# Kernel tuning notes

Hardware: AMD Instinct MI355X
Metric: run time of the kernel (lower is better)

Reference implementation:

```python
import jax, jax.numpy as jnp
import numpy as np

DIM = 512
NUM_HEADS = 16
HEAD_DIM = DIM // NUM_HEADS
RES = (32, 32)
SEQ_SCALE = float(np.log(RES[0] * RES[1]))  # seq_length_scale buffer
TABLE = (2 * RES[0] - 1) * (2 * RES[1] - 1)  # 3969
EPS = 1e-12


def setup_inputs() -> dict:
    key = jax.random.key(0)
    ks = jax.random.split(key, 12)
    B, N, C = 8, RES[0] * RES[1], DIM
    s = 0.02
    return {
        "x": jax.random.normal(ks[0], (B, N, C), dtype=jnp.float32),
        "_h": RES[0],
        "_w": RES[1],
        "relative_pos_index": jax.random.randint(ks[1], (N, N), 0, TABLE, dtype=jnp.int32),
        "relative_coords_table": jax.random.uniform(ks[2], (TABLE, 2), dtype=jnp.float32, minval=-1.0, maxval=1.0),
        "qkv_w": jax.random.normal(ks[3], (3 * C, C), dtype=jnp.float32) * s,
        "qkv_b": jnp.zeros((3 * C,), dtype=jnp.float32),
        "proj_w": jax.random.normal(ks[4], (C, C), dtype=jnp.float32) * s,
        "proj_b": jnp.zeros((C,), dtype=jnp.float32),
        "temperature": jnp.full((NUM_HEADS, 1, 1), float(np.log(np.expm1(1.0 / 0.24))), dtype=jnp.float32),
        "query_embedding": jax.random.normal(ks[5], (NUM_HEADS, 1, HEAD_DIM), dtype=jnp.float32) * s,
        "cpb_fc1_w": jax.random.normal(ks[6], (512, 2), dtype=jnp.float32) * s,
        "cpb_fc1_b": jnp.zeros((512,), dtype=jnp.float32),
        "cpb_fc2_w": jax.random.normal(ks[7], (NUM_HEADS, 512), dtype=jnp.float32) * s,
        "cpb_fc2_b": jnp.zeros((NUM_HEADS,), dtype=jnp.float32),
    }


def _l2norm(t):
    # F.normalize(t, dim=-1): x / max(||x||, eps)
    n = jnp.sqrt(jnp.sum(t * t, axis=-1, keepdims=True))
    return t / jnp.maximum(n, EPS)


def reference(x, _h, _w, relative_pos_index, relative_coords_table,
              qkv_w, qkv_b, proj_w, proj_b, temperature, query_embedding,
              cpb_fc1_w, cpb_fc1_b, cpb_fc2_w, cpb_fc2_b):
    B, N, C = x.shape
    H, hd = NUM_HEADS, HEAD_DIM
    # qkv projection -> [B, N, 3H, hd] -> [B, 3H, N, hd]
    qkv = (x @ qkv_w.T + qkv_b).reshape(B, N, 3 * H, hd).transpose(0, 2, 1, 3)
    q, k, v = jnp.split(qkv, 3, axis=1)  # each [B, H, N, hd]
    # CPB MLP relative bias: [T,2] -> [T,H] -> gather -> [H,N,N]
    t = jax.nn.relu(relative_coords_table @ cpb_fc1_w.T + cpb_fc1_b) @ cpb_fc2_w.T + cpb_fc2_b
    rel_bias = t[relative_pos_index].transpose(2, 0, 1)  # [H, N, N]
    # cosine attention with learned softplus temperature and query embedding
    scale = jax.nn.softplus(temperature) * SEQ_SCALE  # [H,1,1]
    qn = (_l2norm(q) + query_embedding[None]) * scale[None]
    kn = _l2norm(k)
    attn = jnp.einsum('bhnd,bhmd->bhnm', qn, kn) + rel_bias[None]
    attn = jax.nn.softmax(attn, axis=-1)
    out = jnp.einsum('bhnm,bhmd->bhnd', attn, v)  # [B,H,N,hd]
    out = out.transpose(0, 2, 1, 3).reshape(B, N, C)
    return out @ proj_w.T + proj_b
```

## Files before the change

### kernel.cpp

```cpp
#include <hip/hip_runtime.h>
#include <cstdint>
#include <cstddef>

typedef _Float16 f16;
typedef _Float16 f16x4 __attribute__((ext_vector_type(4)));
typedef _Float16 f16x8 __attribute__((ext_vector_type(8)));
typedef float f32x4 __attribute__((ext_vector_type(4)));

#define MFMA32(a,b,c) __builtin_amdgcn_mfma_f32_16x16x32_f16((a),(b),(c),0,0,0)
#define MFMA16(a,b,c) __builtin_amdgcn_mfma_f32_16x16x16f16((a),(b),(c),0,0,0)

__device__ __forceinline__ float fexp2(float x) {
#if __has_builtin(__builtin_amdgcn_exp2f)
  return __builtin_amdgcn_exp2f(x);
#else
  return __expf(x * 0.69314718055994531f);
#endif
}

__device__ __forceinline__ void gload_lds16(const f16* g, f16* l) {
  __builtin_amdgcn_global_load_lds(
      (const __attribute__((address_space(1))) unsigned int*)g,
      (__attribute__((address_space(3))) unsigned int*)l, 16, 0, 0);
}

static constexpr size_t OFF_TCPB = 0;
static constexpr size_t OFF_BIAS = 262144;
static constexpr size_t OFF_XHI  = OFF_BIAS + 33554432;
static constexpr size_t OFF_XLO  = OFF_XHI + 8388608;
static constexpr size_t OFF_WHI  = OFF_XLO + 8388608;
static constexpr size_t OFF_WLO  = OFF_WHI + 1572864;
static constexpr size_t OFF_PW   = OFF_WLO + 1572864;
static constexpr size_t OFF_QHI  = OFF_PW  + 524288;
static constexpr size_t OFF_QLO  = OFF_QHI + 8388608;
static constexpr size_t OFF_KHI  = OFF_QLO + 8388608;
static constexpr size_t OFF_KLO  = OFF_KHI + 8388608;
static constexpr size_t OFF_VT   = OFF_KLO + 8388608;
static constexpr size_t OFF_AO   = OFF_VT  + 8388608;

__global__ __launch_bounds__(256) void k_convert(
    const float* __restrict__ x, const float* __restrict__ qw, const float* __restrict__ pwf,
    f16* __restrict__ xhi, f16* __restrict__ xlo,
    f16* __restrict__ whi, f16* __restrict__ pw)
{
  int i = blockIdx.x * 256 + threadIdx.x;
  const float4* src; f16* dh; f16* dl; int j;
  if (i < 1048576)      { j = i;           src = (const float4*)x;   dh = xhi; dl = xlo; }
  else if (i < 1245184) { j = i - 1048576; src = (const float4*)qw;  dh = whi; dl = nullptr; }
  else                  { j = i - 1245184; src = (const float4*)pwf; dh = pw;  dl = nullptr; }
  float4 v = src[j];
  f16x4 h;
  h[0] = (f16)v.x; h[1] = (f16)v.y; h[2] = (f16)v.z; h[3] = (f16)v.w;
  ((f16x4*)dh)[j] = h;
  if (dl) {
    f16x4 l;
    l[0] = (f16)(v.x - (float)h[0]); l[1] = (f16)(v.y - (float)h[1]);
    l[2] = (f16)(v.z - (float)h[2]); l[3] = (f16)(v.w - (float)h[3]);
    ((f16x4*)dl)[j] = l;
  }
}

__global__ __launch_bounds__(256) void k_cpb(
    const float* __restrict__ table, const float* __restrict__ w1, const float* __restrict__ b1,
    const float* __restrict__ w2, const float* __restrict__ b2, float* __restrict__ t_out)
{
  const int r = blockIdx.x * 4 + (threadIdx.x >> 6);
  const int lane = threadIdx.x & 63;
  if (r >= 3969) return;
  const float c0 = table[2*r], c1 = table[2*r+1];
  const int j0 = lane * 8;
  float h[8];
#pragma unroll
  for (int jj = 0; jj < 8; jj++) {
    int j = j0 + jj;
    float v = c0 * w1[2*j] + c1 * w1[2*j+1] + b1[j];
    h[jj] = v > 0.0f ? v : 0.0f;
  }
  float acc[16];
#pragma unroll
  for (int o = 0; o < 16; o++) {
    const float4* wp = (const float4*)(w2 + o*512 + j0);
    float4 a = wp[0], bb = wp[1];
    acc[o] = a.x*h[0] + a.y*h[1] + a.z*h[2] + a.w*h[3]
           + bb.x*h[4] + bb.y*h[5] + bb.z*h[6] + bb.w*h[7];
  }
#pragma unroll
  for (int o = 0; o < 16; o++) {
    float v = acc[o];
    for (int s = 1; s < 64; s <<= 1) v += __shfl_xor(v, s, 64);
    acc[o] = v;
  }
  if (lane == 0) {
#pragma unroll
    for (int o = 0; o < 16; o++)
      t_out[r*16 + o] = (acc[o] + b2[o]) * 1.4426950408889634f;
  }
}

__global__ __launch_bounds__(256) void k_bias(
    const int* __restrict__ idx, const float* __restrict__ t_cpb, f16* __restrict__ bias_t)
{
  int g = blockIdx.x * 256 + threadIdx.x;
  int n = g & 1023, m4 = g >> 10;
  int4 I = *(const int4*)(idx + (size_t)n*1024 + m4*4);
  int ids[4] = {I.x, I.y, I.z, I.w};
  const float4* T = (const float4*)t_cpb;
#pragma unroll
  for (int half = 0; half < 2; half++) {
    float4 R[4][2];
#pragma unroll
    for (int k = 0; k < 4; k++) {
      R[k][0] = T[ids[k]*4 + half*2];
      R[k][1] = T[ids[k]*4 + half*2 + 1];
    }
#pragma unroll
    for (int hh = 0; hh < 8; hh++) {
      int h = half*8 + hh;
      f16x4 o;
#pragma unroll
      for (int k = 0; k < 4; k++)
        o[k] = (f16)(((const float*)&R[k][hh >> 2])[hh & 3]);
      *(f16x4*)(bias_t + (((size_t)h*256 + m4)*1024 + n)*4) = o;
    }
  }
}

__global__ __launch_bounds__(256) void k_qkv(
    const f16* __restrict__ xhi, const f16* __restrict__ xlo,
    const f16* __restrict__ whi,
    const float* __restrict__ qkvb, const float* __restrict__ temp, const float* __restrict__ qe,
    f16* __restrict__ qh_o, f16* __restrict__ kh_o, f16* __restrict__ vt_o)
{
  __shared__ __align__(16) f16 Ah[8][64][8];
  __shared__ __align__(16) f16 Al[8][64][8];
  __shared__ __align__(16) f16 Bh[8][64][8];
  const int tid = threadIdx.x, lane = tid & 63, w = tid >> 6;
  const int rsel = lane & 15, ksel = lane >> 4;
  const int bx = blockIdx.x & 63, by = blockIdx.x >> 6;
  const int m0 = bx << 7, n0 = by << 7;
  const bool SPLIT = (by < 8);

  const size_t aoff = (size_t)(m0 + w*32 + rsel)*512 + ksel*8;
  const size_t boff = (size_t)(n0 + w*32 + rsel)*512 + ksel*8;
  const f16 *gA0 = xhi + aoff,  *gA1 = gA0 + 16*512;
  const f16 *gAl0 = xlo + aoff, *gAl1 = gAl0 + 16*512;
  const f16 *gB0 = whi + boff,  *gB1 = gB0 + 16*512;
  f16 *lA0 = &Ah[2*w][0][0],  *lA1 = &Ah[2*w+1][0][0];
  f16 *lAl0 = &Al[2*w][0][0], *lAl1 = &Al[2*w+1][0][0];
  f16 *lB0 = &Bh[2*w][0][0],  *lB1 = &Bh[2*w+1][0][0];

  const f32x4 zero = {0.f, 0.f, 0.f, 0.f};
  f32x4 acc[4][4];
#pragma unroll
  for (int mt = 0; mt < 4; mt++)
#pragma unroll
    for (int nt = 0; nt < 4; nt++) acc[mt][nt] = zero;

  const int mb4 = (w & 1) * 4, nb4 = (w >> 1) * 4;
  for (int k0 = 0; k0 < 512; k0 += 32) {
    __syncthreads();
    gload_lds16(gA0 + k0, lA0);
    gload_lds16(gA1 + k0, lA1);
    gload_lds16(gB0 + k0, lB0);
    gload_lds16(gB1 + k0, lB1);
    if (SPLIT) {
      gload_lds16(gAl0 + k0, lAl0);
      gload_lds16(gAl1 + k0, lAl1);
    }
    __syncthreads();
    f16x8 bhf[4];
#pragma unroll
    for (int nt = 0; nt < 4; nt++) bhf[nt] = ((const f16x8*)&Bh[nb4+nt][0][0])[lane];
    if (SPLIT) {
#pragma unroll
      for (int mt = 0; mt < 4; mt++) {
        f16x8 ah = ((const f16x8*)&Ah[mb4+mt][0][0])[lane];
        f16x8 al = ((const f16x8*)&Al[mb4+mt][0][0])[lane];
#pragma unroll
        for (int nt = 0; nt < 4; nt++) {
          acc[mt][nt] = MFMA32(al, bhf[nt], acc[mt][nt]);
          acc[mt][nt] = MFMA32(ah, bhf[nt], acc[mt][nt]);
        }
      }
    } else {
#pragma unroll
      for (int mt = 0; mt < 4; mt++) {
        f16x8 ah = ((const f16x8*)&Ah[mb4+mt][0][0])[lane];
#pragma unroll
        for (int nt = 0; nt < 4; nt++)
          acc[mt][nt] = MFMA32(ah, bhf[nt], acc[mt][nt]);
      }
    }
  }

  const int mbase = m0 + (w & 1)*64, nbase = n0 + (w >> 1)*64;
  float bc[4];
#pragma unroll
  for (int nt = 0; nt < 4; nt++) bc[nt] = qkvb[nbase + nt*16 + rsel];
#pragma unroll
  for (int mt = 0; mt < 4; mt++)
#pragma unroll
    for (int nt = 0; nt < 4; nt++)
#pragma unroll
      for (int r = 0; r < 4; r++) acc[mt][nt][r] += bc[nt];

  if (by < 8) {
    const bool ISQ = (by < 4);
#pragma unroll
    for (int pair = 0; pair < 2; pair++) {
      const int h = ((nbase - (ISQ ? 0 : 512)) >> 5) + pair;
      float sc = 0.f, qe0 = 0.f, qe1 = 0.f;
      if (ISQ) {
        sc  = log1pf(__expf(temp[h])) * 10.0f;
        qe0 = qe[h*32 + rsel];
        qe1 = qe[h*32 + 16 + rsel];
      }
      f16* dh = ISQ ? qh_o : kh_o;
#pragma unroll
      for (int mt = 0; mt < 4; mt++) {
        float ss[4];
#pragma unroll
        for (int r = 0; r < 4; r++) {
          float a = acc[mt][2*pair][r], b = acc[mt][2*pair+1][r];
          ss[r] = a*a + b*b;
        }
        for (int s = 1; s < 16; s <<= 1) {
#pragma unroll
          for (int r = 0; r < 4; r++) ss[r] += __shfl_xor(ss[r], s, 64);
        }
#pragma unroll
        for (int r = 0; r < 4; r++) {
          float rn = 1.0f / fmaxf(sqrtf(ss[r]), 1e-12f);
          int m = mbase + mt*16 + ksel*4 + r;
          int b_ = m >> 10, p = m & 1023;
          size_t base = ((size_t)(b_*16 + h)*1024 + p)*32;
          float v0 = acc[mt][2*pair][r] * rn;
          float v1 = acc[mt][2*pair+1][r] * rn;
          if (ISQ) { v0 = (v0 + qe0) * sc; v1 = (v1 + qe1) * sc; }
          dh[base + rsel]      = (f16)v0;
          dh[base + 16 + rsel] = (f16)v1;
        }
      }
    }
  } else {
#pragma unroll
    for (int mt = 0; mt < 4; mt++) {
      int m = mbase + mt*16 + ksel*4;
      int b_ = m >> 10, p = m & 1023;
#pragma unroll
      for (int nt = 0; nt < 4; nt++) {
        int n = nbase + nt*16 + rsel;
        int g = (n - 1024) >> 5, d = n & 31;
        f16x4 pk;
#pragma unroll
        for (int r = 0; r < 4; r++) pk[r] = (f16)acc[mt][nt][r];
        *(f16x4*)(vt_o + ((size_t)(b_*16 + g)*32 + d)*1024 + p) = pk;
      }
    }
  }
}

__global__ __launch_bounds__(256, 4) void k_attn(
    const f16* __restrict__ qhi, const f16* __restrict__ khi, const f16* __restrict__ vt,
    const f16* __restrict__ bias_t,
    f16* __restrict__ po0, f16* __restrict__ po1,
    float2* __restrict__ ml0, float2* __restrict__ ml1)
{
  __shared__ __align__(16) f16 OT[4][32][40];
  const int lane = threadIdx.x & 63, w = threadIdx.x >> 6;
  const int rsel = lane & 15, ksel = lane >> 4;
  const int bid = blockIdx.x;
  const int xcd = bid & 7;
  const int r1 = bid >> 3;
  const int h = ((r1 & 1) << 3) | xcd;
  const int r2 = r1 >> 1;
  const int qt = r2 & 7, split = (r2 >> 3) & 1, b = r2 >> 4;
  const int bh = b*16 + h;
  const int q0 = qt*128 + w*32;
  const int mstart = split * 512;

  f16x8 Qh[2];
#pragma unroll
  for (int c = 0; c < 2; c++)
    Qh[c] = *(const f16x8*)(qhi + ((size_t)bh*1024 + q0 + c*16 + rsel)*32 + ksel*8);

  const char* kb = (const char*)(khi + (size_t)bh*32768);
  const char* vb = (const char*)(vt  + (size_t)bh*32768);
  const char* bb = (const char*)(bias_t + (size_t)h*1048576);
  int kOff = ((mstart + rsel)*32 + ksel*8) * 2;
  int vOff = (rsel*1024 + mstart + ksel*4) * 2;
  int bOff = (((mstart >> 2) + ksel)*1024 + q0 + rsel) * 8;

  f32x4 O[2][2];
  float mi[2], li[2];
#pragma unroll
  for (int c = 0; c < 2; c++) {
    O[c][0] = (f32x4){0.f,0.f,0.f,0.f};
    O[c][1] = (f32x4){0.f,0.f,0.f,0.f};
    mi[c] = -3.0e38f; li[c] = 0.f;
  }

  f16x8 Kn0 = *(const f16x8*)(kb + kOff);
  f16x8 Kn1 = *(const f16x8*)(kb + kOff + 1024);
  kOff += 2048;

  for (int it = 0; it < 16; ++it) {
    f16x8 K0 = Kn0, K1 = Kn1;
    if (it < 15) {
      Kn0 = *(const f16x8*)(kb + kOff);
      Kn1 = *(const f16x8*)(kb + kOff + 1024);
      kOff += 2048;
    }
    f16x4 Va[2][2];
    Va[0][0] = *(const f16x4*)(vb + vOff);
    Va[1][0] = *(const f16x4*)(vb + vOff + 32);
    Va[0][1] = *(const f16x4*)(vb + vOff + 32768);
    Va[1][1] = *(const f16x4*)(vb + vOff + 32800);
    vOff += 64;
    f16x4 Bb[2][2];
    Bb[0][0] = *(const f16x4*)(bb + bOff);
    Bb[0][1] = *(const f16x4*)(bb + bOff + 128);
    Bb[1][0] = *(const f16x4*)(bb + bOff + 32768);
    Bb[1][1] = *(const f16x4*)(bb + bOff + 32896);
    bOff += 65536;

    f32x4 St[2][2];
#pragma unroll
    for (int f = 0; f < 2; f++)
#pragma unroll
      for (int c = 0; c < 2; c++) {
        f32x4 Ci;
#pragma unroll
        for (int r = 0; r < 4; r++) Ci[r] = (float)Bb[f][c][r];
        St[f][c] = MFMA32(f ? K1 : K0, Qh[c], Ci);
      }

    f16x4 P16[2][2];
#pragma unroll
    for (int c = 0; c < 2; c++) {
      float cm = fmaxf(fmaxf(fmaxf(St[0][c][0], St[0][c][1]), fmaxf(St[0][c][2], St[0][c][3])),
                       fmaxf(fmaxf(St[1][c][0], St[1][c][1]), fmaxf(St[1][c][2], St[1][c][3])));
      cm = fmaxf(cm, __shfl_xor(cm, 16, 64));
      cm = fmaxf(cm, __shfl_xor(cm, 32, 64));
      float mn = fmaxf(mi[c], cm);
      float alpha = fexp2(mi[c] - mn);
      mi[c] = mn;
      float rs = 0.f;
#pragma unroll
      for (int f = 0; f < 2; f++)
#pragma unroll
        for (int r = 0; r < 4; r++) {
          float p = fexp2(St[f][c][r] - mn);
          rs += p;
          P16[f][c][r] = (f16)p;
        }
      li[c] = li[c]*alpha + rs;
#pragma unroll
      for (int dt = 0; dt < 2; dt++)
#pragma unroll
        for (int r = 0; r < 4; r++) O[c][dt][r] *= alpha;
    }
#pragma unroll
    for (int c = 0; c < 2; c++)
#pragma unroll
      for (int dt = 0; dt < 2; dt++) {
        O[c][dt] = MFMA16(Va[0][dt], P16[0][c], O[c][dt]);
        O[c][dt] = MFMA16(Va[1][dt], P16[1][c], O[c][dt]);
      }
  }

#pragma unroll
  for (int c = 0; c < 2; c++) {
    li[c] += __shfl_xor(li[c], 16, 64);
    li[c] += __shfl_xor(li[c], 32, 64);
    float inv = 1.0f / li[c];
#pragma unroll
    for (int dt = 0; dt < 2; dt++)
#pragma unroll
      for (int r = 0; r < 4; r++)
        OT[w][c*16 + rsel][dt*16 + ksel*4 + r] = (f16)(O[c][dt][r] * inv);
  }
  f16* po_s = split ? po1 : po0;
  float2* ml_s = split ? ml1 : ml0;
  int row = lane >> 1, half = lane & 1;
  f16x8 o0 = *(const f16x8*)(&OT[w][row][half*16]);
  f16x8 o1 = *(const f16x8*)(&OT[w][row][half*16 + 8]);
  f16* outp = po_s + ((size_t)bh*1024 + q0 + row)*32 + half*16;
  *(f16x8*)outp = o0;
  *(f16x8*)(outp + 8) = o1;
  if (lane < 32) {
    int c = lane >> 4;
    float mm = c ? mi[1] : mi[0];
    float ll = c ? li[1] : li[0];
    ml_s[(size_t)bh*1024 + q0 + lane] = make_float2(mm, ll);
  }
}

__global__ __launch_bounds__(256) void k_merge(
    const f16* __restrict__ po0, const f16* __restrict__ po1,
    const float2* __restrict__ ml0, const float2* __restrict__ ml1,
    f16* __restrict__ ao)
{
  int tid = blockIdx.x * 256 + threadIdx.x;
  int h = tid & 15, q = (tid >> 4) & 1023, b = tid >> 14;
  int bh = b*16 + h;
  size_t rec = (size_t)bh*1024 + q;
  float2 a = ml0[rec], c = ml1[rec];
  float M = fmaxf(a.x, c.x);
  float w0 = a.y * fexp2(a.x - M);
  float w1 = c.y * fexp2(c.x - M);
  float inv = 1.0f / (w0 + w1);
  w0 *= inv; w1 *= inv;
  const f16x8* p0 = (const f16x8*)(po0 + rec*32);
  const f16x8* p1 = (const f16x8*)(po1 + rec*32);
  f16* op = ao + ((size_t)b*1024 + q)*512 + h*32;
#pragma unroll
  for (int i = 0; i < 4; i++) {
    f16x8 x0 = p0[i], x1 = p1[i];
    f16x8 o;
#pragma unroll
    for (int j = 0; j < 8; j++) o[j] = (f16)((float)x0[j]*w0 + (float)x1[j]*w1);
    ((f16x8*)op)[i] = o;
  }
}

__global__ __launch_bounds__(256) void k_proj(
    const f16* __restrict__ A, const f16* __restrict__ Bw,
    const float* __restrict__ pb, float* __restrict__ out)
{
  __shared__ __align__(16) f16 Ah[8][64][8];
  __shared__ __align__(16) f16 Bh[8][64][8];
  const int tid = threadIdx.x, lane = tid & 63, w = tid >> 6;
  const int rsel = lane & 15, ksel = lane >> 4;
  const int bx = blockIdx.x & 63, by = blockIdx.x >> 6;
  const int m0 = bx << 7, n0 = by << 7;
  const f16 *gA0 = A + (size_t)(m0 + w*32 + rsel)*512 + ksel*8,  *gA1 = gA0 + 16*512;
  const f16 *gB0 = Bw + (size_t)(n0 + w*32 + rsel)*512 + ksel*8, *gB1 = gB0 + 16*512;
  f16 *lA0 = &Ah[2*w][0][0], *lA1 = &Ah[2*w+1][0][0];
  f16 *lB0 = &Bh[2*w][0][0], *lB1 = &Bh[2*w+1][0][0];
  const f32x4 zero = {0.f, 0.f, 0.f, 0.f};
  f32x4 acc[4][4];
#pragma unroll
  for (int mt = 0; mt < 4; mt++)
#pragma unroll
    for (int nt = 0; nt < 4; nt++) acc[mt][nt] = zero;
  const int mb4 = (w & 1)*4, nb4 = (w >> 1)*4;
  for (int k0 = 0; k0 < 512; k0 += 32) {
    __syncthreads();
    gload_lds16(gA0 + k0, lA0);
    gload_lds16(gA1 + k0, lA1);
    gload_lds16(gB0 + k0, lB0);
    gload_lds16(gB1 + k0, lB1);
    __syncthreads();
    f16x8 bhf[4];
#pragma unroll
    for (int nt = 0; nt < 4; nt++) bhf[nt] = ((const f16x8*)&Bh[nb4+nt][0][0])[lane];
#pragma unroll
    for (int mt = 0; mt < 4; mt++) {
      f16x8 ah = ((const f16x8*)&Ah[mb4+mt][0][0])[lane];
#pragma unroll
      for (int nt = 0; nt < 4; nt++)
        acc[mt][nt] = MFMA32(ah, bhf[nt], acc[mt][nt]);
    }
  }
  const int mbase = m0 + (w & 1)*64, nbase = n0 + (w >> 1)*64;
  float bc[4];
#pragma unroll
  for (int nt = 0; nt < 4; nt++) bc[nt] = pb[nbase + nt*16 + rsel];
#pragma unroll
  for (int mt = 0; mt < 4; mt++)
#pragma unroll
    for (int nt = 0; nt < 4; nt++)
#pragma unroll
      for (int r = 0; r < 4; r++)
        out[(size_t)(mbase + mt*16 + ksel*4 + r)*512 + nbase + nt*16 + rsel] =
            acc[mt][nt][r] + bc[nt];
}

extern "C" void kernel_launch(void* const* d_in, const int* in_sizes, int n_in,
                              void* d_out, int out_size, void* d_ws, size_t ws_size,
                              hipStream_t stream) {
  const float* x    = (const float*)d_in[0];
  const int*   rpi  = (const int*)d_in[3];
  const float* rct  = (const float*)d_in[4];
  const float* qw   = (const float*)d_in[5];
  const float* qb   = (const float*)d_in[6];
  const float* pwf  = (const float*)d_in[7];
  const float* pbv  = (const float*)d_in[8];
  const float* temp = (const float*)d_in[9];
  const float* qe   = (const float*)d_in[10];
  const float* f1w  = (const float*)d_in[11];
  const float* f1b  = (const float*)d_in[12];
  const float* f2w  = (const float*)d_in[13];
  const float* f2b  = (const float*)d_in[14];

  char* ws = (char*)d_ws;
  float* t_cpb  = (float*)(ws + OFF_TCPB);
  f16* bias_t   = (f16*)(ws + OFF_BIAS);
  f16* xhi = (f16*)(ws + OFF_XHI);
  f16* xlo = (f16*)(ws + OFF_XLO);
  f16* whi = (f16*)(ws + OFF_WHI);
  f16* pw  = (f16*)(ws + OFF_PW);
  f16* qhi = (f16*)(ws + OFF_QHI);
  f16* khi = (f16*)(ws + OFF_KHI);
  f16* vt  = (f16*)(ws + OFF_VT);
  f16* ao  = (f16*)(ws + OFF_AO);
  f16* po0 = (f16*)(ws + OFF_KLO);
  f16* po1 = (f16*)(ws + OFF_XHI);
  float2* ml0 = (float2*)(ws + OFF_XLO);
  float2* ml1 = ml0 + 131072;

  k_convert<<<5120, 256, 0, stream>>>(x, qw, pwf, xhi, xlo, whi, pw);
  k_cpb<<<993, 256, 0, stream>>>(rct, f1w, f1b, f2w, f2b, t_cpb);
  k_bias<<<1024, 256, 0, stream>>>(rpi, t_cpb, bias_t);
  k_qkv<<<768, 256, 0, stream>>>(xhi, xlo, whi, qb, temp, qe, qhi, khi, vt);
  k_attn<<<2048, 256, 0, stream>>>(qhi, khi, vt, bias_t, po0, po1, ml0, ml1);
  k_merge<<<512, 256, 0, stream>>>(po0, po1, ml0, ml1, ao);
  k_proj<<<256, 256, 0, stream>>>(ao, pw, pbv, (float*)d_out);
}
```

Measured before the change: 288.8 us.

## Use two-pass softmax: precompute row max, drop online rescaling

Replaces the online-softmax loop with two passes over the key range. The first pass computes QK^T plus bias only to find the exact row max. The second pass recomputes the scores, exponentiates against that fixed max and accumulates P·V with no per-iteration alpha rescale or cross-lane max shuffles. This removes the serial shuffle/rescale dependency chain, but it doubles the QK MFMAs and the K and bias loads, and it drops the software prefetch of K.

```diff
diff --git a/kernel.cpp b/kernel.cpp
--- a/kernel.cpp
+++ b/kernel.cpp
@@ -286,87 +286,85 @@
 
   const char* kb = (const char*)(khi + (size_t)bh*32768);
   const char* vb = (const char*)(vt  + (size_t)bh*32768);
-  const char* bb = (const char*)(bias_t + (size_t)h*1048576);
-  int kOff = ((mstart + rsel)*32 + ksel*8) * 2;
-  int vOff = (rsel*1024 + mstart + ksel*4) * 2;
-  int bOff = (((mstart >> 2) + ksel)*1024 + q0 + rsel) * 8;
+  const char* bbp = (const char*)(bias_t + (size_t)h*1048576);
+  const int kOff0 = ((mstart + rsel)*32 + ksel*8) * 2;
+  const int vOff0 = (rsel*1024 + mstart + ksel*4) * 2;
+  const int bOff0 = (((mstart >> 2) + ksel)*1024 + q0 + rsel) * 8;
+
+  float mx[2] = {-3.0e38f, -3.0e38f};
+  {
+    int kOff = kOff0, bOff = bOff0;
+    for (int it = 0; it < 16; ++it) {
+      f16x8 K0 = *(const f16x8*)(kb + kOff);
+      f16x8 K1 = *(const f16x8*)(kb + kOff + 1024);
+      f16x4 Bb[2][2];
+      Bb[0][0] = *(const f16x4*)(bbp + bOff);
+      Bb[0][1] = *(const f16x4*)(bbp + bOff + 128);
+      Bb[1][0] = *(const f16x4*)(bbp + bOff + 32768);
+      Bb[1][1] = *(const f16x4*)(bbp + bOff + 32896);
+      kOff += 2048; bOff += 65536;
+#pragma unroll
+      for (int f = 0; f < 2; f++)
+#pragma unroll
+        for (int c = 0; c < 2; c++) {
+          f32x4 Ci;
+#pragma unroll
+          for (int r = 0; r < 4; r++) Ci[r] = (float)Bb[f][c][r];
+          f32x4 St = MFMA32(f ? K1 : K0, Qh[c], Ci);
+          mx[c] = fmaxf(mx[c], fmaxf(fmaxf(St[0], St[1]), fmaxf(St[2], St[3])));
+        }
+    }
+  }
+#pragma unroll
+  for (int c = 0; c < 2; c++) {
+    mx[c] = fmaxf(mx[c], __shfl_xor(mx[c], 16, 64));
+    mx[c] = fmaxf(mx[c], __shfl_xor(mx[c], 32, 64));
+  }
 
   f32x4 O[2][2];
-  float mi[2], li[2];
-#pragma unroll
-  for (int c = 0; c < 2; c++) {
-    O[c][0] = (f32x4){0.f,0.f,0.f,0.f};
-    O[c][1] = (f32x4){0.f,0.f,0.f,0.f};
-    mi[c] = -3.0e38f; li[c] = 0.f;
-  }
-
-  f16x8 Kn0 = *(const f16x8*)(kb + kOff);
-  f16x8 Kn1 = *(const f16x8*)(kb + kOff + 1024);
-  kOff += 2048;
-
-  for (int it = 0; it < 16; ++it) {
-    f16x8 K0 = Kn0, K1 = Kn1;
-    if (it < 15) {
-      Kn0 = *(const f16x8*)(kb + kOff);
-      Kn1 = *(const f16x8*)(kb + kOff + 1024);
-      kOff += 2048;
-    }
-    f16x4 Va[2][2];
-    Va[0][0] = *(const f16x4*)(vb + vOff);
-    Va[1][0] = *(const f16x4*)(vb + vOff + 32);
-    Va[0][1] = *(const f16x4*)(vb + vOff + 32768);
-    Va[1][1] = *(const f16x4*)(vb + vOff + 32800);
-    vOff += 64;
-    f16x4 Bb[2][2];
-    Bb[0][0] = *(const f16x4*)(bb + bOff);
-    Bb[0][1] = *(const f16x4*)(bb + bOff + 128);
-    Bb[1][0] = *(const f16x4*)(bb + bOff + 32768);
-    Bb[1][1] = *(const f16x4*)(bb + bOff + 32896);
-    bOff += 65536;
-
-    f32x4 St[2][2];
-#pragma unroll
-    for (int f = 0; f < 2; f++)
-#pragma unroll
-      for (int c = 0; c < 2; c++) {
-        f32x4 Ci;
-#pragma unroll
-        for (int r = 0; r < 4; r++) Ci[r] = (float)Bb[f][c][r];
-        St[f][c] = MFMA32(f ? K1 : K0, Qh[c], Ci);
-      }
-
-    f16x4 P16[2][2];
-#pragma unroll
-    for (int c = 0; c < 2; c++) {
-      float cm = fmaxf(fmaxf(fmaxf(St[0][c][0], St[0][c][1]), fmaxf(St[0][c][2], St[0][c][3])),
-                       fmaxf(fmaxf(St[1][c][0], St[1][c][1]), fmaxf(St[1][c][2], St[1][c][3])));
-      cm = fmaxf(cm, __shfl_xor(cm, 16, 64));
-      cm = fmaxf(cm, __shfl_xor(cm, 32, 64));
-      float mn = fmaxf(mi[c], cm);
-      float alpha = fexp2(mi[c] - mn);
-      mi[c] = mn;
-      float rs = 0.f;
+  float li[2] = {0.f, 0.f};
+  O[0][0] = (f32x4){0.f,0.f,0.f,0.f}; O[0][1] = O[0][0];
+  O[1][0] = O[0][0]; O[1][1] = O[0][0];
+  {
+    int kOff = kOff0, vOff = vOff0, bOff = bOff0;
+    for (int it = 0; it < 16; ++it) {
+      f16x8 K0 = *(const f16x8*)(kb + kOff);
+      f16x8 K1 = *(const f16x8*)(kb + kOff + 1024);
+      f16x4 Va[2][2], Bb[2][2];
+      Va[0][0] = *(const f16x4*)(vb + vOff);
+      Va[1][0] = *(const f16x4*)(vb + vOff + 32);
+      Va[0][1] = *(const f16x4*)(vb + vOff + 32768);
+      Va[1][1] = *(const f16x4*)(vb + vOff + 32800);
+      Bb[0][0] = *(const f16x4*)(bbp + bOff);
+      Bb[0][1] = *(const f16x4*)(bbp + bOff + 128);
+      Bb[1][0] = *(const f16x4*)(bbp + bOff + 32768);
+      Bb[1][1] = *(const f16x4*)(bbp + bOff + 32896);
+      kOff += 2048; vOff += 64; bOff += 65536;
+
+      f16x4 P16[2][2];
 #pragma unroll
       for (int f = 0; f < 2; f++)
 #pragma unroll
-        for (int r = 0; r < 4; r++) {
-          float p = fexp2(St[f][c][r] - mn);
-          rs += p;
-          P16[f][c][r] = (f16)p;
-        }
-      li[c] = li[c]*alpha + rs;
-#pragma unroll
-      for (int dt = 0; dt < 2; dt++)
-#pragma unroll
-        for (int r = 0; r < 4; r++) O[c][dt][r] *= alpha;
-    }
-#pragma unroll
-    for (int c = 0; c < 2; c++)
-#pragma unroll
-      for (int dt = 0; dt < 2; dt++) {
-        O[c][dt] = MFMA16(Va[0][dt], P16[0][c], O[c][dt]);
-        O[c][dt] = MFMA16(Va[1][dt], P16[1][c], O[c][dt]);
-      }
+        for (int c = 0; c < 2; c++) {
+          f32x4 Ci;
+#pragma unroll
+          for (int r = 0; r < 4; r++) Ci[r] = (float)Bb[f][c][r];
+          f32x4 St = MFMA32(f ? K1 : K0, Qh[c], Ci);
+#pragma unroll
+          for (int r = 0; r < 4; r++) {
+            float p = fexp2(St[r] - mx[c]);
+            li[c] += p;
+            P16[f][c][r] = (f16)p;
+          }
+        }
+#pragma unroll
+      for (int c = 0; c < 2; c++)
+#pragma unroll
+        for (int dt = 0; dt < 2; dt++) {
+          O[c][dt] = MFMA16(Va[0][dt], P16[0][c], O[c][dt]);
+          O[c][dt] = MFMA16(Va[1][dt], P16[1][c], O[c][dt]);
+        }
+    }
   }
 
 #pragma unroll
@@ -390,7 +388,7 @@
   *(f16x8*)(outp + 8) = o1;
   if (lane < 32) {
     int c = lane >> 4;
-    float mm = c ? mi[1] : mi[0];
+    float mm = c ? mx[1] : mx[0];
     float ll = c ? li[1] : li[0];
     ml_s[(size_t)bh*1024 + q0 + lane] = make_float2(mm, ll);
   }
```

After: 316.8 us. +9.7%, slower.

## Split attention keys across waves in-block and merge partials in LDS

Applied to the files above, without the earlier changes.

Restructures attention so each block handles 32 queries and its four waves each process a quarter of the keys. The waves' partial outputs and max/sum statistics are combined in shared memory, which removes the separate merge kernel and its global round trip. The online-softmax rescale is skipped when no lane's running max changes, and the K prefetch is removed. The cost is more blocks (4096), Q loads repeated per wave, a block barrier, and less latency hiding without the prefetch.

```diff
diff --git a/kernel.cpp b/kernel.cpp
--- a/kernel.cpp
+++ b/kernel.cpp
@@ -262,22 +262,22 @@
 
 __global__ __launch_bounds__(256, 4) void k_attn(
     const f16* __restrict__ qhi, const f16* __restrict__ khi, const f16* __restrict__ vt,
-    const f16* __restrict__ bias_t,
-    f16* __restrict__ po0, f16* __restrict__ po1,
-    float2* __restrict__ ml0, float2* __restrict__ ml1)
-{
-  __shared__ __align__(16) f16 OT[4][32][40];
+    const f16* __restrict__ bias_t, f16* __restrict__ ao)
+{
+  __shared__ __align__(16) f16 OT[4][32][36];
+  __shared__ __align__(16) float2 ML[4][32];
   const int lane = threadIdx.x & 63, w = threadIdx.x >> 6;
   const int rsel = lane & 15, ksel = lane >> 4;
   const int bid = blockIdx.x;
   const int xcd = bid & 7;
   const int r1 = bid >> 3;
-  const int h = ((r1 & 1) << 3) | xcd;
-  const int r2 = r1 >> 1;
-  const int qt = r2 & 7, split = (r2 >> 3) & 1, b = r2 >> 4;
+  const int qt = r1 & 31;
+  const int r2 = r1 >> 5;
+  const int hHi = r2 & 1, b = r2 >> 1;
+  const int h = (hHi << 3) | xcd;
   const int bh = b*16 + h;
-  const int q0 = qt*128 + w*32;
-  const int mstart = split * 512;
+  const int q0 = qt*32;
+  const int mstart = w*256;
 
   f16x8 Qh[2];
 #pragma unroll
@@ -286,7 +286,7 @@
 
   const char* kb = (const char*)(khi + (size_t)bh*32768);
   const char* vb = (const char*)(vt  + (size_t)bh*32768);
-  const char* bb = (const char*)(bias_t + (size_t)h*1048576);
+  const char* bbp = (const char*)(bias_t + (size_t)h*1048576);
   int kOff = ((mstart + rsel)*32 + ksel*8) * 2;
   int vOff = (rsel*1024 + mstart + ksel*4) * 2;
   int bOff = (((mstart >> 2) + ksel)*1024 + q0 + rsel) * 8;
@@ -300,29 +300,19 @@
     mi[c] = -3.0e38f; li[c] = 0.f;
   }
 
-  f16x8 Kn0 = *(const f16x8*)(kb + kOff);
-  f16x8 Kn1 = *(const f16x8*)(kb + kOff + 1024);
-  kOff += 2048;
-
-  for (int it = 0; it < 16; ++it) {
-    f16x8 K0 = Kn0, K1 = Kn1;
-    if (it < 15) {
-      Kn0 = *(const f16x8*)(kb + kOff);
-      Kn1 = *(const f16x8*)(kb + kOff + 1024);
-      kOff += 2048;
-    }
-    f16x4 Va[2][2];
+  for (int it = 0; it < 8; ++it) {
+    f16x8 K0 = *(const f16x8*)(kb + kOff);
+    f16x8 K1 = *(const f16x8*)(kb + kOff + 1024);
+    f16x4 Va[2][2], Bb[2][2];
     Va[0][0] = *(const f16x4*)(vb + vOff);
     Va[1][0] = *(const f16x4*)(vb + vOff + 32);
     Va[0][1] = *(const f16x4*)(vb + vOff + 32768);
     Va[1][1] = *(const f16x4*)(vb + vOff + 32800);
-    vOff += 64;
-    f16x4 Bb[2][2];
-    Bb[0][0] = *(const f16x4*)(bb + bOff);
-    Bb[0][1] = *(const f16x4*)(bb + bOff + 128);
-    Bb[1][0] = *(const f16x4*)(bb + bOff + 32768);
-    Bb[1][1] = *(const f16x4*)(bb + bOff + 32896);
-    bOff += 65536;
+    Bb[0][0] = *(const f16x4*)(bbp + bOff);
+    Bb[0][1] = *(const f16x4*)(bbp + bOff + 128);
+    Bb[1][0] = *(const f16x4*)(bbp + bOff + 32768);
+    Bb[1][1] = *(const f16x4*)(bbp + bOff + 32896);
+    kOff += 2048; vOff += 64; bOff += 65536;
 
     f32x4 St[2][2];
 #pragma unroll
@@ -342,9 +332,8 @@
                        fmaxf(fmaxf(St[1][c][0], St[1][c][1]), fmaxf(St[1][c][2], St[1][c][3])));
       cm = fmaxf(cm, __shfl_xor(cm, 16, 64));
       cm = fmaxf(cm, __shfl_xor(cm, 32, 64));
-      float mn = fmaxf(mi[c], cm);
-      float alpha = fexp2(mi[c] - mn);
-      mi[c] = mn;
+      bool upd = cm > mi[c];
+      float mn = upd ? cm : mi[c];
       float rs = 0.f;
 #pragma unroll
       for (int f = 0; f < 2; f++)
@@ -354,11 +343,17 @@
           rs += p;
           P16[f][c][r] = (f16)p;
         }
-      li[c] = li[c]*alpha + rs;
-#pragma unroll
-      for (int dt = 0; dt < 2; dt++)
-#pragma unroll
-        for (int r = 0; r < 4; r++) O[c][dt][r] *= alpha;
+      if (__ballot(upd)) {
+        float alpha = fexp2(mi[c] - mn);
+        mi[c] = mn;
+        li[c] = li[c]*alpha + rs;
+#pragma unroll
+        for (int dt = 0; dt < 2; dt++)
+#pragma unroll
+          for (int r = 0; r < 4; r++) O[c][dt][r] *= alpha;
+      } else {
+        li[c] += rs;
+      }
     }
 #pragma unroll
     for (int c = 0; c < 2; c++)
@@ -379,48 +374,29 @@
 #pragma unroll
       for (int r = 0; r < 4; r++)
         OT[w][c*16 + rsel][dt*16 + ksel*4 + r] = (f16)(O[c][dt][r] * inv);
-  }
-  f16* po_s = split ? po1 : po0;
-  float2* ml_s = split ? ml1 : ml0;
-  int row = lane >> 1, half = lane & 1;
-  f16x8 o0 = *(const f16x8*)(&OT[w][row][half*16]);
-  f16x8 o1 = *(const f16x8*)(&OT[w][row][half*16 + 8]);
-  f16* outp = po_s + ((size_t)bh*1024 + q0 + row)*32 + half*16;
-  *(f16x8*)outp = o0;
-  *(f16x8*)(outp + 8) = o1;
-  if (lane < 32) {
-    int c = lane >> 4;
-    float mm = c ? mi[1] : mi[0];
-    float ll = c ? li[1] : li[0];
-    ml_s[(size_t)bh*1024 + q0 + lane] = make_float2(mm, ll);
-  }
-}
-
-__global__ __launch_bounds__(256) void k_merge(
-    const f16* __restrict__ po0, const f16* __restrict__ po1,
-    const float2* __restrict__ ml0, const float2* __restrict__ ml1,
-    f16* __restrict__ ao)
-{
-  int tid = blockIdx.x * 256 + threadIdx.x;
-  int h = tid & 15, q = (tid >> 4) & 1023, b = tid >> 14;
-  int bh = b*16 + h;
-  size_t rec = (size_t)bh*1024 + q;
-  float2 a = ml0[rec], c = ml1[rec];
-  float M = fmaxf(a.x, c.x);
-  float w0 = a.y * fexp2(a.x - M);
-  float w1 = c.y * fexp2(c.x - M);
-  float inv = 1.0f / (w0 + w1);
-  w0 *= inv; w1 *= inv;
-  const f16x8* p0 = (const f16x8*)(po0 + rec*32);
-  const f16x8* p1 = (const f16x8*)(po1 + rec*32);
-  f16* op = ao + ((size_t)b*1024 + q)*512 + h*32;
-#pragma unroll
-  for (int i = 0; i < 4; i++) {
-    f16x8 x0 = p0[i], x1 = p1[i];
-    f16x8 o;
-#pragma unroll
-    for (int j = 0; j < 8; j++) o[j] = (f16)((float)x0[j]*w0 + (float)x1[j]*w1);
-    ((f16x8*)op)[i] = o;
+    if (ksel == 0) ML[w][c*16 + rsel] = make_float2(mi[c], li[c]);
+  }
+  __syncthreads();
+
+  {
+    int t = threadIdx.x;
+    int q = t >> 3, dg = t & 7;
+    float2 m0_ = ML[0][q], m1_ = ML[1][q], m2_ = ML[2][q], m3_ = ML[3][q];
+    float M = fmaxf(fmaxf(m0_.x, m1_.x), fmaxf(m2_.x, m3_.x));
+    float w0 = m0_.y * fexp2(m0_.x - M);
+    float w1 = m1_.y * fexp2(m1_.x - M);
+    float w2 = m2_.y * fexp2(m2_.x - M);
+    float w3 = m3_.y * fexp2(m3_.x - M);
+    float inv = 1.0f / (w0 + w1 + w2 + w3);
+    f16x4 p0 = *(const f16x4*)(&OT[0][q][dg*4]);
+    f16x4 p1 = *(const f16x4*)(&OT[1][q][dg*4]);
+    f16x4 p2 = *(const f16x4*)(&OT[2][q][dg*4]);
+    f16x4 p3 = *(const f16x4*)(&OT[3][q][dg*4]);
+    f16x4 o;
+#pragma unroll
+    for (int r = 0; r < 4; r++)
+      o[r] = (f16)(((float)p0[r]*w0 + (float)p1[r]*w1 + (float)p2[r]*w2 + (float)p3[r]*w3) * inv);
+    *(f16x4*)(ao + ((size_t)b*1024 + q0 + q)*512 + h*32 + dg*4) = o;
   }
 }
 
@@ -505,16 +481,11 @@
   f16* khi = (f16*)(ws + OFF_KHI);
   f16* vt  = (f16*)(ws + OFF_VT);
   f16* ao  = (f16*)(ws + OFF_AO);
-  f16* po0 = (f16*)(ws + OFF_KLO);
-  f16* po1 = (f16*)(ws + OFF_XHI);
-  float2* ml0 = (float2*)(ws + OFF_XLO);
-  float2* ml1 = ml0 + 131072;
 
   k_convert<<<5120, 256, 0, stream>>>(x, qw, pwf, xhi, xlo, whi, pw);
   k_cpb<<<993, 256, 0, stream>>>(rct, f1w, f1b, f2w, f2b, t_cpb);
   k_bias<<<1024, 256, 0, stream>>>(rpi, t_cpb, bias_t);
   k_qkv<<<768, 256, 0, stream>>>(xhi, xlo, whi, qb, temp, qe, qhi, khi, vt);
-  k_attn<<<2048, 256, 0, stream>>>(qhi, khi, vt, bias_t, po0, po1, ml0, ml1);
-  k_merge<<<512, 256, 0, stream>>>(po0, po1, ml0, ml1, ao);
+  k_attn<<<4096, 256, 0, stream>>>(qhi, khi, vt, bias_t, ao);
   k_proj<<<256, 256, 0, stream>>>(ao, pw, pbv, (float*)d_out);
 }
```

Measured after the change: 282.9 us. -2.0%, faster.
